# Performance work log

Hardware: AMD Instinct MI355X
Metric: run time of the kernel (lower is better)

The kernel has to match this reference:

```python
import jax, jax.numpy as jnp
import numpy as np

C = 256          # C_in == C_out
G = C // 4       # groups = C_in/4 -> 4 channels per group
K = 3
STRIDE = 1
PAD = 2
DIL = 2
EPS = 1e-5

@jax.custom_vjp
def binarize(x):
    # 1-bit sign binarization with straight-through estimator (STE)
    return jnp.sign(x)

def _bin_fwd(x):
    return jnp.sign(x), x

def _bin_bwd(x, g):
    # STE with hardtanh clip: pass grad where |x| <= 1
    return (g * (jnp.abs(x) <= 1.0).astype(g.dtype),)

binarize.defvjp(_bin_fwd, _bin_bwd)

def setup_inputs() -> dict:
    key = jax.random.key(0)
    k1, k2, k3, k4, k5, k6 = jax.random.split(key, 6)
    x = jax.random.normal(k1, (64, C, 32, 32), jnp.float32)
    # grouped conv weight: [C_out, C_in/groups, K, K] = [256, 4, 3, 3]
    weight = jax.random.normal(k2, (C, C // G, K, K), jnp.float32) * 0.1
    gamma = 1.0 + 0.1 * jax.random.normal(k3, (C,), jnp.float32)
    beta = 0.1 * jax.random.normal(k4, (C,), jnp.float32)
    running_mean = 0.1 * jax.random.normal(k5, (C,), jnp.float32)
    running_var = jax.random.uniform(k6, (C,), jnp.float32, 0.5, 1.5)
    return {"x": x, "weight": weight, "gamma": gamma, "beta": beta,
            "running_mean": running_mean, "running_var": running_var}

def reference(x, weight, gamma, beta, running_mean, running_var):
    # BatchNorm2d (inference form with running stats)
    inv = gamma * jax.lax.rsqrt(running_var + EPS)            # [C]
    h = x * inv[None, :, None, None] + (beta - running_mean * inv)[None, :, None, None]
    # binarize activations and weights (1w1a)
    a = binarize(h)
    w = binarize(weight)
    # grouped dilated conv, stride 1, pad 2, dilation 2 -> same HxW
    out = jax.lax.conv_general_dilated(
        a, w,
        window_strides=(STRIDE, STRIDE),
        padding=[(PAD, PAD), (PAD, PAD)],
        rhs_dilation=(DIL, DIL),
        dimension_numbers=("NCHW", "OIHW", "NCHW"),
        feature_group_count=G)
    # channel shuffle: [N,C,H,W] -> [N,g,C/g,H,W] -> [N,C/g,g,H,W] -> [N,C,H,W]
    N, Cc, H, W = out.shape
    out = out.reshape(N, G, Cc // G, H, W).transpose(0, 2, 1, 3, 4).reshape(N, Cc, H, W)
    # identity shortcut (stride == 1)
    return out + x
```

## Files before the change

kernel.cpp:

```cpp
#include <hip/hip_runtime.h>

#ifndef __has_builtin
#define __has_builtin(x) 0
#endif

#if __has_builtin(__builtin_amdgcn_sdot4)
#define DOT4(a, b, c) __builtin_amdgcn_sdot4((a), (b), (c), false)
#else
__device__ __forceinline__ int dot4_sw(int a, int b, int c) {
#pragma unroll
    for (int k = 0; k < 4; ++k)
        c += (int)(signed char)((a >> (8 * k)) & 0xff) *
             (int)(signed char)((b >> (8 * k)) & 0xff);
    return c;
}
#define DOT4(a, b, c) dot4_sw((a), (b), (c))
#endif

constexpr int CH   = 256;
constexpr int NPIX = 1024;
constexpr float BN_EPS = 1e-5f;

__device__ __forceinline__ float rfl_f(float v) {
    return __int_as_float(__builtin_amdgcn_readfirstlane(__float_as_int(v)));
}

__global__ __launch_bounds__(256, 4)
void bconv(const float* __restrict__ x,
           const float* __restrict__ wgt,
           const float* __restrict__ gamma,
           const float* __restrict__ beta,
           const float* __restrict__ rmean,
           const float* __restrict__ rvar,
           float* __restrict__ out) {
    __shared__ int   wq_lds[36];
    __shared__ float bn_lds[8];

    const int tid  = threadIdx.x;
    const int n0   = (blockIdx.x >> 6) * 2;
    const int g    = blockIdx.x & 63;
    const int pix0 = tid * 4;
    const int row  = pix0 >> 5;
    const int col0 = pix0 & 31;
    const float* xnA = x + n0 * CH * NPIX;
    const float* xnB = xnA + CH * NPIX;
    float* onA = out + n0 * CH * NPIX;
    float* onB = onA + CH * NPIX;

    float4 xv[3][4];
    auto load_xv = [&](const float* xn) {
#pragma unroll
        for (int kh = 0; kh < 3; ++kh) {
            const int rs  = row + 2 * kh - 2;
            const int rsc = min(max(rs, 0), 31);
            const float* rp = xn + g * 4 * NPIX + rsc * 32 + col0;
#pragma unroll
            for (int ci = 0; ci < 4; ++ci)
                xv[kh][ci] = *(const float4*)(rp + ci * NPIX);
        }
    };

    load_xv(xnA);
    float4 scA[4];
#pragma unroll
    for (int c2 = 0; c2 < 4; ++c2)
        scA[c2] = *(const float4*)(xnA + (c2 * 64 + g) * NPIX + pix0);

    if (tid < 144) {
        const int c2 = tid / 36, r = tid % 36, ci = r / 9, tap = r % 9;
        float w = wgt[g * 144 + tid];
        int s = (w > 0.f) ? 1 : ((w < 0.f) ? -1 : 0);
        ((char*)wq_lds)[(c2 * 9 + tap) * 4 + ci] = (char)s;
    } else if (tid < 148) {
        const int ci = tid - 144, c = g * 4 + ci;
        float r  = __fdiv_rn(1.0f, __fsqrt_rn(__fadd_rn(rvar[c], BN_EPS)));
        float iv = __fmul_rn(gamma[c], r);
        bn_lds[ci]     = iv;
        bn_lds[4 + ci] = __fsub_rn(beta[c], __fmul_rn(rmean[c], iv));
    }
    __syncthreads();

    int wq[4][9];
#pragma unroll
    for (int c2 = 0; c2 < 4; ++c2)
#pragma unroll
        for (int t = 0; t < 9; ++t)
            wq[c2][t] = __builtin_amdgcn_readfirstlane(wq_lds[c2 * 9 + t]);
    float inv[4], bias[4];
#pragma unroll
    for (int ci = 0; ci < 4; ++ci) {
        inv[ci]  = rfl_f(bn_lds[ci]);
        bias[ci] = rfl_f(bn_lds[4 + ci]);
    }

    auto pack = [&](int pkc[3][4]) {
#pragma unroll
        for (int kh = 0; kh < 3; ++kh) {
            const bool ok = (unsigned)(row + 2 * kh - 2) < 32u;
#pragma unroll
            for (int p = 0; p < 4; ++p) {
                int v = 0;
#pragma unroll
                for (int ci = 0; ci < 4; ++ci) {
                    float h = __fadd_rn(__fmul_rn(((const float*)&xv[kh][ci])[p], inv[ci]), bias[ci]);
                    int s = (h > 0.f) ? 1 : ((h < 0.f) ? -1 : 0);
                    v |= (s & 0xff) << (8 * ci);
                }
                pkc[kh][p] = ok ? v : 0;
            }
        }
    };

    const bool le = (col0 == 0), re = (col0 == 28);
    auto compute_store = [&](const int pkc[3][4], const float4 sc[4], float* on) {
        int a[3][8];
#pragma unroll
        for (int kh = 0; kh < 3; ++kh) {
            int l2 = __shfl_up(pkc[kh][2], 1);
            int l3 = __shfl_up(pkc[kh][3], 1);
            int r0 = __shfl_down(pkc[kh][0], 1);
            int r1 = __shfl_down(pkc[kh][1], 1);
            a[kh][0] = le ? 0 : l2;
            a[kh][1] = le ? 0 : l3;
            a[kh][2] = pkc[kh][0]; a[kh][3] = pkc[kh][1];
            a[kh][4] = pkc[kh][2]; a[kh][5] = pkc[kh][3];
            a[kh][6] = re ? 0 : r0;
            a[kh][7] = re ? 0 : r1;
        }
#pragma unroll
        for (int c2 = 0; c2 < 4; ++c2) {
            float4 o;
#pragma unroll
            for (int p = 0; p < 4; ++p) {
                int acc = 0;
#pragma unroll
                for (int kh = 0; kh < 3; ++kh)
#pragma unroll
                    for (int kw = 0; kw < 3; ++kw)
                        acc = DOT4(a[kh][p + 2 * kw], wq[c2][kh * 3 + kw], acc);
                ((float*)&o)[p] = __fadd_rn((float)acc, ((const float*)&sc[c2])[p]);
            }
            *(float4*)(on + (c2 * 64 + g) * NPIX + pix0) = o;
        }
    };

    int pkcA[3][4];
    pack(pkcA);

    load_xv(xnB);

    compute_store(pkcA, scA, onA);

    int pkcB[3][4];
    pack(pkcB);

    float4 scB[4];
#pragma unroll
    for (int c2 = 0; c2 < 4; ++c2)
        scB[c2] = *(const float4*)(xnB + (c2 * 64 + g) * NPIX + pix0);

    compute_store(pkcB, scB, onB);
}

extern "C" void kernel_launch(void* const* d_in, const int* in_sizes, int n_in,
                              void* d_out, int out_size, void* d_ws, size_t ws_size,
                              hipStream_t stream) {
    const float* x     = (const float*)d_in[0];
    const float* wgt   = (const float*)d_in[1];
    const float* gamma = (const float*)d_in[2];
    const float* beta  = (const float*)d_in[3];
    const float* rmean = (const float*)d_in[4];
    const float* rvar  = (const float*)d_in[5];
    float* out = (float*)d_out;

    const int N = in_sizes[0] / (CH * NPIX);
    bconv<<<(N / 2) * 64, 256, 0, stream>>>(x, wgt, gamma, beta, rmean, rvar, out);
}
```

Baseline: 33.77 us.

## Pack binarized activations into LDS and gather halo rows instead of reloading

Each thread now loads only its own 4 channels' pixel rows once, binarizes and packs them into an LDS tile, and the 3x3 dilated halo is gathered from LDS rather than reloading three row-shifted copies of x from global memory and using lane shuffles. Both images' inputs and shortcuts are loaded up front to expose memory parallelism, and BN parameters are computed per-thread instead of via LDS broadcast. This cuts global load volume roughly threefold for the conv input. The cost is about 8 KB of LDS, extra barriers, and more live registers, which may lower occupancy.

Measured after the change: 34.95 us. 3.5% more time.

```diff
diff --git a/kernel.cpp b/kernel.cpp
--- a/kernel.cpp
+++ b/kernel.cpp
@@ -19,6 +19,7 @@
 
 constexpr int CH   = 256;
 constexpr int NPIX = 1024;
+constexpr int LW   = 33;
 constexpr float BN_EPS = 1e-5f;
 
 __device__ __forceinline__ float rfl_f(float v) {
@@ -33,6 +34,7 @@
            const float* __restrict__ rmean,
            const float* __restrict__ rvar,
            float* __restrict__ out) {
+    __shared__ int   pk_lds[2][32][LW];
     __shared__ int   wq_lds[36];
     __shared__ float bn_lds[8];
 
@@ -47,24 +49,19 @@
     float* onA = out + n0 * CH * NPIX;
     float* onB = onA + CH * NPIX;
 
-    float4 xv[3][4];
-    auto load_xv = [&](const float* xn) {
+    float4 xvA[4], scA[4], xvB[4], scB[4];
 #pragma unroll
-        for (int kh = 0; kh < 3; ++kh) {
-            const int rs  = row + 2 * kh - 2;
-            const int rsc = min(max(rs, 0), 31);
-            const float* rp = xn + g * 4 * NPIX + rsc * 32 + col0;
-#pragma unroll
-            for (int ci = 0; ci < 4; ++ci)
-                xv[kh][ci] = *(const float4*)(rp + ci * NPIX);
-        }
-    };
-
-    load_xv(xnA);
-    float4 scA[4];
+    for (int ci = 0; ci < 4; ++ci)
+        xvA[ci] = *(const float4*)(xnA + (g * 4 + ci) * NPIX + pix0);
 #pragma unroll
     for (int c2 = 0; c2 < 4; ++c2)
         scA[c2] = *(const float4*)(xnA + (c2 * 64 + g) * NPIX + pix0);
+#pragma unroll
+    for (int ci = 0; ci < 4; ++ci)
+        xvB[ci] = *(const float4*)(xnB + (g * 4 + ci) * NPIX + pix0);
+#pragma unroll
+    for (int c2 = 0; c2 < 4; ++c2)
+        scB[c2] = *(const float4*)(xnB + (c2 * 64 + g) * NPIX + pix0);
 
     if (tid < 144) {
         const int c2 = tid / 36, r = tid % 36, ci = r / 9, tap = r % 9;
@@ -78,6 +75,31 @@
         bn_lds[ci]     = iv;
         bn_lds[4 + ci] = __fsub_rn(beta[c], __fmul_rn(rmean[c], iv));
     }
+
+    float inv[4], bias[4];
+#pragma unroll
+    for (int ci = 0; ci < 4; ++ci) {
+        const int c = g * 4 + ci;
+        float r  = __fdiv_rn(1.0f, __fsqrt_rn(__fadd_rn(rvar[c], BN_EPS)));
+        inv[ci]  = __fmul_rn(gamma[c], r);
+        bias[ci] = __fsub_rn(beta[c], __fmul_rn(rmean[c], inv[ci]));
+    }
+
+    auto pack_to_lds = [&](const float4 xv[4], int img) {
+#pragma unroll
+        for (int p = 0; p < 4; ++p) {
+            int v = 0;
+#pragma unroll
+            for (int ci = 0; ci < 4; ++ci) {
+                float h = __fadd_rn(__fmul_rn(((const float*)&xv[ci])[p], inv[ci]), bias[ci]);
+                int s = (h > 0.f) ? 1 : ((h < 0.f) ? -1 : 0);
+                v |= (s & 0xff) << (8 * ci);
+            }
+            pk_lds[img][row][col0 + p] = v;
+        }
+    };
+
+    pack_to_lds(xvA, 0);
     __syncthreads();
 
     int wq[4][9];
@@ -86,50 +108,29 @@
 #pragma unroll
         for (int t = 0; t < 9; ++t)
             wq[c2][t] = __builtin_amdgcn_readfirstlane(wq_lds[c2 * 9 + t]);
-    float inv[4], bias[4];
-#pragma unroll
-    for (int ci = 0; ci < 4; ++ci) {
-        inv[ci]  = rfl_f(bn_lds[ci]);
-        bias[ci] = rfl_f(bn_lds[4 + ci]);
-    }
 
-    auto pack = [&](int pkc[3][4]) {
+    const bool le = (col0 == 0), re = (col0 == 28);
+
+    auto gather = [&](int img, int a[3][8]) {
 #pragma unroll
         for (int kh = 0; kh < 3; ++kh) {
-            const bool ok = (unsigned)(row + 2 * kh - 2) < 32u;
+            const int rs  = row + 2 * kh - 2;
+            const int rr  = min(max(rs, 0), 31);
+            const bool okr = (unsigned)rs < 32u;
 #pragma unroll
-            for (int p = 0; p < 4; ++p) {
-                int v = 0;
-#pragma unroll
-                for (int ci = 0; ci < 4; ++ci) {
-                    float h = __fadd_rn(__fmul_rn(((const float*)&xv[kh][ci])[p], inv[ci]), bias[ci]);
-                    int s = (h > 0.f) ? 1 : ((h < 0.f) ? -1 : 0);
-                    v |= (s & 0xff) << (8 * ci);
-                }
-                pkc[kh][p] = ok ? v : 0;
+            for (int j = 0; j < 8; ++j) {
+                const int c  = col0 - 2 + j;
+                const int cc = min(max(c, 0), 31);
+                const bool okc = !(j < 2 && le) && !(j > 5 && re);
+                int v = pk_lds[img][rr][cc];
+                a[kh][j] = (okr && okc) ? v : 0;
             }
         }
     };
 
-    const bool le = (col0 == 0), re = (col0 == 28);
-    auto compute_store = [&](const int pkc[3][4], const float4 sc[4], float* on) {
-        int a[3][8];
+    auto compute = [&](const int a[3][8], const float4 sc[4], float4 o[4]) {
 #pragma unroll
-        for (int kh = 0; kh < 3; ++kh) {
-            int l2 = __shfl_up(pkc[kh][2], 1);
-            int l3 = __shfl_up(pkc[kh][3], 1);
-            int r0 = __shfl_down(pkc[kh][0], 1);
-            int r1 = __shfl_down(pkc[kh][1], 1);
-            a[kh][0] = le ? 0 : l2;
-            a[kh][1] = le ? 0 : l3;
-            a[kh][2] = pkc[kh][0]; a[kh][3] = pkc[kh][1];
-            a[kh][4] = pkc[kh][2]; a[kh][5] = pkc[kh][3];
-            a[kh][6] = re ? 0 : r0;
-            a[kh][7] = re ? 0 : r1;
-        }
-#pragma unroll
-        for (int c2 = 0; c2 < 4; ++c2) {
-            float4 o;
+        for (int c2 = 0; c2 < 4; ++c2)
 #pragma unroll
             for (int p = 0; p < 4; ++p) {
                 int acc = 0;
@@ -138,28 +139,29 @@
 #pragma unroll
                     for (int kw = 0; kw < 3; ++kw)
                         acc = DOT4(a[kh][p + 2 * kw], wq[c2][kh * 3 + kw], acc);
-                ((float*)&o)[p] = __fadd_rn((float)acc, ((const float*)&sc[c2])[p]);
+                ((float*)&o[c2])[p] = __fadd_rn((float)acc, ((const float*)&sc[c2])[p]);
             }
-            *(float4*)(on + (c2 * 64 + g) * NPIX + pix0) = o;
-        }
     };
 
-    int pkcA[3][4];
-    pack(pkcA);
+    int aA[3][8];
+    gather(0, aA);
+    float4 oA[4];
+    compute(aA, scA, oA);
 
-    load_xv(xnB);
+    pack_to_lds(xvB, 1);
+    __syncthreads();
 
-    compute_store(pkcA, scA, onA);
-
-    int pkcB[3][4];
-    pack(pkcB);
-
-    float4 scB[4];
 #pragma unroll
     for (int c2 = 0; c2 < 4; ++c2)
-        scB[c2] = *(const float4*)(xnB + (c2 * 64 + g) * NPIX + pix0);
+        *(float4*)(onA + (c2 * 64 + g) * NPIX + pix0) = oA[c2];
 
-    compute_store(pkcB, scB, onB);
+    int aB[3][8];
+    gather(1, aB);
+    float4 oB[4];
+    compute(aB, scB, oB);
+#pragma unroll
+    for (int c2 = 0; c2 < 4; ++c2)
+        *(float4*)(onB + (c2 * 64 + g) * NPIX + pix0) = oB[c2];
 }
 
 extern "C" void kernel_launch(void* const* d_in, const int* in_sizes, int n_in,
```
